# Kernel optimization log

Measured on AMD Instinct MI355X. Metric: run time of the kernel, lower is better.

The kernel has to match this reference:

```python
import jax, jax.numpy as jnp
import numpy as np

N, F, DE = 768, 64, 32
H0, H1, H2, OUT = 64, 64, 128, 1  # hidden_dim=[64,64,128], output_dim=1


def _mlp(x, Wa, ba, Wb, bb):
    # two Dense layers with relu, as in the repo's MLP
    h = jax.nn.relu(x @ Wa + ba)
    return jax.nn.relu(h @ Wb + bb)


def _edge_conv_e(A, x, e, Wa, ba, Wb, bb):
    # EdgeConvE: per-edge message MLP([x_i, x_j - x_i, e_ij]) aggregated
    # over neighbors j weighted by the (binary) adjacency.
    n = x.shape[0]
    xi = jnp.broadcast_to(x[:, None, :], (n, n, x.shape[1]))  # [N,N,F]
    xj = jnp.broadcast_to(x[None, :, :], (n, n, x.shape[1]))  # [N,N,F]
    feat = jnp.concatenate([xi, xj - xi, e], axis=-1)         # [N,N,2F+De]
    m = _mlp(feat, Wa, ba, Wb, bb)                            # [N,N,H]
    return jnp.einsum('ij,ijh->ih', A, m)                     # scatter-sum over j


def setup_inputs() -> dict:
    key = jax.random.key(0)
    ks = jax.random.split(key, 16)
    adj = (jax.random.uniform(ks[0], (N, N)) < 0.05).astype(jnp.float32)
    x = jax.random.normal(ks[1], (N, F), dtype=jnp.float32)
    e = jax.random.normal(ks[2], (N, N, DE), dtype=jnp.float32)
    s = 0.05
    d_in1 = 2 * F + DE          # 160
    d_in2 = 2 * H0 + DE         # 160
    return {
        'ajacency': adj,
        'node_features': x,
        'edge_attributes': e,
        'W1a': jax.random.normal(ks[3], (d_in1, H0)) * s, 'b1a': jnp.zeros((H0,)),
        'W1b': jax.random.normal(ks[4], (H0, H0)) * s,    'b1b': jnp.zeros((H0,)),
        'W2a': jax.random.normal(ks[5], (d_in2, H1)) * s, 'b2a': jnp.zeros((H1,)),
        'W2b': jax.random.normal(ks[6], (H1, H0)) * s,    'b2b': jnp.zeros((H0,)),
        'W3': jax.random.normal(ks[7], (H0, H2)) * s,     'b3': jnp.zeros((H2,)),
        'W4': jax.random.normal(ks[8], (H2, OUT)) * s,    'b4': jnp.zeros((OUT,)),
    }


def reference(ajacency, node_features, edge_attributes,
              W1a, b1a, W1b, b1b, W2a, b2a, W2b, b2b, W3, b3, W4, b4):
    x = _edge_conv_e(ajacency, node_features, edge_attributes, W1a, b1a, W1b, b1b)
    x = _edge_conv_e(ajacency, x, edge_attributes, W2a, b2a, W2b, b2b)
    x = jax.nn.relu(x @ W3 + b3)
    return jax.nn.sigmoid(x @ W4 + b4)  # [N, OUT]
```

## Files before the change

### kernel.cpp

```cpp
#include <hip/hip_runtime.h>
#include <math.h>


#define NN 768
#define FF 64
#define DE 32
#define HH 64
#define CAP 128
#define SH1S 72

using bf16x8 = __attribute__((ext_vector_type(8))) short;
using f32x4  = __attribute__((ext_vector_type(4))) float;

__device__ __forceinline__ short f2b(float f) {
  unsigned u = __float_as_uint(f);
  return (short)((u + 0x7fffu + ((u >> 16) & 1u)) >> 16);
}

__device__ __forceinline__ void phaseB(
    const short* sh1b, const short* __restrict__ Wbp,
    const float* __restrict__ bb, float* xrow, int c, int lane, int wv)
{
  if (c > 0) {
    const int nt = (c + 15) >> 4;
    const int q = lane >> 4, n = lane & 15;
    bf16x8 b0 = *(const bf16x8*)(Wbp + (((wv * 2 + 0) * 4 + q) * 16 + n) * 8);
    bf16x8 b1 = *(const bf16x8*)(Wbp + (((wv * 2 + 1) * 4 + q) * 16 + n) * 8);
    const float bias = bb[wv * 16 + n];
    float s = 0.0f;
    for (int rt = 0; rt < nt; ++rt) {
      const short* sa = sh1b + (rt * 16 + n) * SH1S + q * 8;
      bf16x8 a0 = *(const bf16x8*)(sa);
      bf16x8 a1 = *(const bf16x8*)(sa + 32);
      f32x4 acc = {0.f, 0.f, 0.f, 0.f};
      acc = __builtin_amdgcn_mfma_f32_16x16x32_bf16(a0, b0, acc, 0, 0, 0);
      acc = __builtin_amdgcn_mfma_f32_16x16x32_bf16(a1, b1, acc, 0, 0, 0);
#pragma unroll
      for (int reg = 0; reg < 4; ++reg) {
        const int row = rt * 16 + q * 4 + reg;
        const float v = fmaxf(acc[reg] + bias, 0.0f);
        s += (row < c) ? v : 0.0f;
      }
    }
    s += __shfl_down(s, 32);
    s += __shfl_down(s, 16);
    if (lane < 16) xrow[wv * 16 + lane] = s;
  } else {
    if (lane < 16) xrow[wv * 16 + lane] = 0.0f;
  }
}

__device__ __forceinline__ void phaseA(
    int i, int c, const int* s_j, const float* __restrict__ e,
    const float* __restrict__ U, const float* __restrict__ V,
    const short* __restrict__ Wep, short (*esb)[DE], short* sh1b,
    int tid, int lane, int wv)
{
  for (int slot = tid >> 3; slot < c; slot += 32) {
    const int j = s_j[slot];
    float4 f = ((const float4*)(e + ((size_t)i * NN + j) * DE))[tid & 7];
    short4 s4 = { f2b(f.x), f2b(f.y), f2b(f.z), f2b(f.w) };
    *(short4*)(&esb[slot][(tid & 7) * 4]) = s4;
  }

  const int q = lane >> 4, n = lane & 15;
  const int ch = wv * 16 + n;
  bf16x8 bwe = *(const bf16x8*)(Wep + ((wv * 4 + q) * 16 + n) * 8);
  const float u_ch = (c > 0) ? U[(i << 6) + ch] : 0.0f;
  __syncthreads();

  const int nt = (c + 15) >> 4;
  for (int rt = 0; rt < nt; ++rt) {
    bf16x8 a = *(const bf16x8*)(&esb[rt * 16 + n][q * 8]);
    f32x4 P = {0.f, 0.f, 0.f, 0.f};
    P = __builtin_amdgcn_mfma_f32_16x16x32_bf16(a, bwe, P, 0, 0, 0);
#pragma unroll
    for (int reg = 0; reg < 4; ++reg) {
      const int slot = rt * 16 + q * 4 + reg;
      short val = 0;
      if (slot < c) {
        const int j = s_j[slot];
        val = f2b(fmaxf(u_ch + V[(j << 6) + ch] + P[reg], 0.0f));
      }
      sh1b[slot * SH1S + ch] = val;
    }
  }
  __syncthreads();
}

__global__ __launch_bounds__(256) void scan_kernel(
    const float* __restrict__ A, const float* __restrict__ x,
    const float* __restrict__ W, const float* __restrict__ bias,
    const float* __restrict__ We1, const float* __restrict__ We2,
    const float* __restrict__ Wb1, const float* __restrict__ Wb2,
    int* __restrict__ cnt, int* __restrict__ jl,
    float* __restrict__ U, float* __restrict__ V,
    short* __restrict__ Wbp1, short* __restrict__ Wbp2,
    short* __restrict__ We1p, short* __restrict__ We2p)
{
  const int i = blockIdx.x;
  const int tid = threadIdx.x;
  __shared__ int s_cnt;
  __shared__ int s_j[CAP];
  __shared__ float sx[64];
  __shared__ float su[4][64], sv[4][64];

  if (tid == 0) s_cnt = 0;
  __syncthreads();
  if (tid < 64) sx[tid] = x[i * 64 + tid];
  if (tid < NN / 4) {
    float4 a = ((const float4*)(A + i * NN))[tid];
    if (a.x != 0.0f) { int p = atomicAdd(&s_cnt, 1); if (p < CAP) s_j[p] = tid * 4 + 0; }
    if (a.y != 0.0f) { int p = atomicAdd(&s_cnt, 1); if (p < CAP) s_j[p] = tid * 4 + 1; }
    if (a.z != 0.0f) { int p = atomicAdd(&s_cnt, 1); if (p < CAP) s_j[p] = tid * 4 + 2; }
    if (a.w != 0.0f) { int p = atomicAdd(&s_cnt, 1); if (p < CAP) s_j[p] = tid * 4 + 3; }
  }

  if (i < 2) {
    const float* srcb = (i == 0) ? Wb1 : Wb2;
    short* dstb = (i == 0) ? Wbp1 : Wbp2;
    for (int L = tid; L < 4096; L += 256) {
      const int j = L & 7, n = (L >> 3) & 15, quad = (L >> 7) & 3;
      const int kb = (L >> 9) & 1, ct = L >> 10;
      dstb[L] = f2b(srcb[(kb * 32 + quad * 8 + j) * 64 + ct * 16 + n]);
    }
    const float* srce = (i == 0) ? We1 : We2;
    short* dste = (i == 0) ? We1p : We2p;
    for (int L = tid; L < 2048; L += 256) {
      const int j = L & 7, n = (L >> 3) & 15, q = (L >> 7) & 3, ct = L >> 9;
      dste[L] = f2b(srce[(q * 8 + j) * 64 + ct * 16 + n]);
    }
  }
  __syncthreads();
  const int c = min(s_cnt, CAP);

  const int c64 = tid & 63, sg = tid >> 6;
  {
    float u = 0.0f, v = 0.0f;
#pragma unroll
    for (int t = 0; t < 16; ++t) {
      const int d = sg * 16 + t;
      const float xv = sx[d];
      const float wxi = W[d * 64 + c64];
      const float wxj = W[(64 + d) * 64 + c64];
      u = fmaf(xv, wxi - wxj, u);
      v = fmaf(xv, wxj, v);
    }
    su[sg][c64] = u; sv[sg][c64] = v;
  }
  __syncthreads();

  if (tid < 64) {
    U[i * 64 + tid] = su[0][tid] + su[1][tid] + su[2][tid] + su[3][tid] + bias[tid];
    V[i * 64 + tid] = sv[0][tid] + sv[1][tid] + sv[2][tid] + sv[3][tid];
  }
  if (tid == 0) cnt[i] = c;
  for (int t = tid; t < c; t += 256) jl[(i << 7) + t] = s_j[t];
}

__global__ __launch_bounds__(256) void conv1uv2_kernel(
    const int* __restrict__ cnt, const int* __restrict__ jl,
    const float* __restrict__ e,
    const float* __restrict__ U1, const float* __restrict__ V1,
    const short* __restrict__ We1p, const short* __restrict__ Wbp1,
    const float* __restrict__ b1b,
    const float* __restrict__ W2a, const float* __restrict__ b2a,
    float* __restrict__ U2, float* __restrict__ V2)
{
  const int i = blockIdx.x;
  const int tid = threadIdx.x, lane = tid & 63, wv = tid >> 6;
  __shared__ __align__(16) short esb[CAP][DE];
  __shared__ __align__(16) short sh1b[CAP * SH1S];
  __shared__ int s_j[CAP];
  __shared__ float xrow[64];
  __shared__ float su[4][64], sv[4][64];

  const int c = cnt[i];
  for (int t = tid; t < c; t += 256) s_j[t] = jl[(i << 7) + t];
  __syncthreads();

  phaseA(i, c, s_j, e, U1, V1, We1p, esb, sh1b, tid, lane, wv);
  phaseB(sh1b, Wbp1, b1b, xrow, c, lane, wv);
  __syncthreads();

  const int c64 = tid & 63, qr = tid >> 6;
  {
    float u = 0.0f, v = 0.0f;
#pragma unroll
    for (int t = 0; t < 16; ++t) {
      const int d = qr * 16 + t;
      const float xv = xrow[d];
      const float wxi = W2a[d * 64 + c64];
      const float wxj = W2a[(64 + d) * 64 + c64];
      u = fmaf(xv, wxi - wxj, u);
      v = fmaf(xv, wxj, v);
    }
    su[qr][c64] = u; sv[qr][c64] = v;
  }
  __syncthreads();
  if (tid < 64) {
    U2[i * 64 + tid] = su[0][tid] + su[1][tid] + su[2][tid] + su[3][tid] + b2a[tid];
    V2[i * 64 + tid] = sv[0][tid] + sv[1][tid] + sv[2][tid] + sv[3][tid];
  }
}

__global__ __launch_bounds__(256) void conv2head_kernel(
    const int* __restrict__ cnt, const int* __restrict__ jl,
    const float* __restrict__ e,
    const float* __restrict__ U2, const float* __restrict__ V2,
    const short* __restrict__ We2p, const short* __restrict__ Wbp2,
    const float* __restrict__ b2b,
    const float* __restrict__ W3, const float* __restrict__ b3,
    const float* __restrict__ W4, const float* __restrict__ b4,
    float* __restrict__ out)
{
  const int i = blockIdx.x;
  const int tid = threadIdx.x, lane = tid & 63, wv = tid >> 6;
  __shared__ __align__(16) short esb[CAP][DE];
  __shared__ __align__(16) short sh1b[CAP * SH1S];
  __shared__ int s_j[CAP];
  __shared__ float xrow[64];
  __shared__ float sred[2];

  const int c = cnt[i];
  for (int t = tid; t < c; t += 256) s_j[t] = jl[(i << 7) + t];
  __syncthreads();

  phaseA(i, c, s_j, e, U2, V2, We2p, esb, sh1b, tid, lane, wv);
  phaseB(sh1b, Wbp2, b2b, xrow, c, lane, wv);
  __syncthreads();

  if (tid < 128) {
    float p = b3[tid];
#pragma unroll
    for (int cc = 0; cc < 64; ++cc) p = fmaf(xrow[cc], W3[cc * 128 + tid], p);
    p = fmaxf(p, 0.0f);
    float v = p * W4[tid];
    v += __shfl_down(v, 32);
    v += __shfl_down(v, 16);
    v += __shfl_down(v, 8);
    v += __shfl_down(v, 4);
    v += __shfl_down(v, 2);
    v += __shfl_down(v, 1);
    if (lane == 0) sred[wv] = v;
  }
  __syncthreads();
  if (tid == 0) {
    const float z = sred[0] + sred[1] + b4[0];
    out[i] = 1.0f / (1.0f + expf(-z));
  }
}

extern "C" void kernel_launch(void* const* d_in, const int* in_sizes, int n_in,
                              void* d_out, int out_size, void* d_ws, size_t ws_size,
                              hipStream_t stream) {
  const float* A   = (const float*)d_in[0];
  const float* x   = (const float*)d_in[1];
  const float* e   = (const float*)d_in[2];
  const float* W1a = (const float*)d_in[3];
  const float* b1a = (const float*)d_in[4];
  const float* W1b = (const float*)d_in[5];
  const float* b1b = (const float*)d_in[6];
  const float* W2a = (const float*)d_in[7];
  const float* b2a = (const float*)d_in[8];
  const float* W2b = (const float*)d_in[9];
  const float* b2b = (const float*)d_in[10];
  const float* W3  = (const float*)d_in[11];
  const float* b3  = (const float*)d_in[12];
  const float* W4  = (const float*)d_in[13];
  const float* b4  = (const float*)d_in[14];
  float* out = (float*)d_out;

  int*   cnt  = (int*)d_ws;
  int*   jl   = cnt + NN;
  float* U1   = (float*)(jl + NN * CAP);
  float* V1   = U1 + NN * HH;
  float* U2   = V1 + NN * HH;
  float* V2   = U2 + NN * HH;
  short* Wbp1 = (short*)(V2 + NN * HH);
  short* Wbp2 = Wbp1 + 4096;
  short* We1p = Wbp2 + 4096;
  short* We2p = We1p + 2048;

  scan_kernel<<<NN, 256, 0, stream>>>(A, x, W1a, b1a,
                                      W1a + 128 * HH, W2a + 128 * HH,
                                      W1b, W2b,
                                      cnt, jl, U1, V1, Wbp1, Wbp2, We1p, We2p);
  conv1uv2_kernel<<<NN, 256, 0, stream>>>(cnt, jl, e, U1, V1, We1p, Wbp1, b1b,
                                          W2a, b2a, U2, V2);
  conv2head_kernel<<<NN, 256, 0, stream>>>(cnt, jl, e, U2, V2, We2p, Wbp2, b2b,
                                           W3, b3, W4, b4, out);
}
```

Baseline: 149.9 us.

## Split U/V and weight packing into small kernel, fuse adjacency scan into conv1

Computes the first-layer U/V projections and the bf16 weight packing in a separate, smaller kernel of NN/4+2 blocks, with each thread doing a full 64-term dot product. The adjacency scan moves into the first conv kernel, which now writes cnt and jl itself instead of reading them back from global memory. This cuts the dependency on a full 768-block scan pass and removes one round trip of the neighbor list. In exchange each conv1 block does its scan serially before phase A.

```diff
diff --git a/kernel.cpp b/kernel.cpp
--- a/kernel.cpp
+++ b/kernel.cpp
@@ -88,26 +88,74 @@
   __syncthreads();
 }
 
-__global__ __launch_bounds__(256) void scan_kernel(
-    const float* __restrict__ A, const float* __restrict__ x,
-    const float* __restrict__ W, const float* __restrict__ bias,
+__global__ __launch_bounds__(256) void uvpack_kernel(
+    const float* __restrict__ x, const float* __restrict__ W,
+    const float* __restrict__ bias,
     const float* __restrict__ We1, const float* __restrict__ We2,
     const float* __restrict__ Wb1, const float* __restrict__ Wb2,
-    int* __restrict__ cnt, int* __restrict__ jl,
     float* __restrict__ U, float* __restrict__ V,
     short* __restrict__ Wbp1, short* __restrict__ Wbp2,
     short* __restrict__ We1p, short* __restrict__ We2p)
 {
+  const int b = blockIdx.x;
+  const int tid = threadIdx.x;
+
+  if (b >= NN / 4) {
+    const int which = b - NN / 4;
+    const float* srcb = (which == 0) ? Wb1 : Wb2;
+    short* dstb = (which == 0) ? Wbp1 : Wbp2;
+    for (int L = tid; L < 4096; L += 256) {
+      const int j = L & 7, n = (L >> 3) & 15, quad = (L >> 7) & 3;
+      const int kb = (L >> 9) & 1, ct = L >> 10;
+      dstb[L] = f2b(srcb[(kb * 32 + quad * 8 + j) * 64 + ct * 16 + n]);
+    }
+    const float* srce = (which == 0) ? We1 : We2;
+    short* dste = (which == 0) ? We1p : We2p;
+    for (int L = tid; L < 2048; L += 256) {
+      const int j = L & 7, n = (L >> 3) & 15, q = (L >> 7) & 3, ct = L >> 9;
+      dste[L] = f2b(srce[(q * 8 + j) * 64 + ct * 16 + n]);
+    }
+    return;
+  }
+
+  const int rr = tid >> 6, c64 = tid & 63;
+  const int r = b * 4 + rr;
+  __shared__ float sx[4][64];
+  sx[rr][c64] = x[r * 64 + c64];
+  __syncthreads();
+  float u = bias[c64], v = 0.0f;
+#pragma unroll
+  for (int d = 0; d < 64; ++d) {
+    const float xv = sx[rr][d];
+    const float wxi = W[d * 64 + c64];
+    const float wxj = W[(64 + d) * 64 + c64];
+    u = fmaf(xv, wxi - wxj, u);
+    v = fmaf(xv, wxj, v);
+  }
+  U[r * 64 + c64] = u;
+  V[r * 64 + c64] = v;
+}
+
+__global__ __launch_bounds__(256) void scanconv1_kernel(
+    const float* __restrict__ A, const float* __restrict__ e,
+    const float* __restrict__ U1, const float* __restrict__ V1,
+    const short* __restrict__ We1p, const short* __restrict__ Wbp1,
+    const float* __restrict__ b1b,
+    const float* __restrict__ W2a, const float* __restrict__ b2a,
+    int* __restrict__ cnt, int* __restrict__ jl,
+    float* __restrict__ U2, float* __restrict__ V2)
+{
   const int i = blockIdx.x;
-  const int tid = threadIdx.x;
+  const int tid = threadIdx.x, lane = tid & 63, wv = tid >> 6;
   __shared__ int s_cnt;
   __shared__ int s_j[CAP];
-  __shared__ float sx[64];
+  __shared__ __align__(16) short esb[CAP][DE];
+  __shared__ __align__(16) short sh1b[CAP * SH1S];
+  __shared__ float xrow[64];
   __shared__ float su[4][64], sv[4][64];
 
   if (tid == 0) s_cnt = 0;
   __syncthreads();
-  if (tid < 64) sx[tid] = x[i * 64 + tid];
   if (tid < NN / 4) {
     float4 a = ((const float4*)(A + i * NN))[tid];
     if (a.x != 0.0f) { int p = atomicAdd(&s_cnt, 1); if (p < CAP) s_j[p] = tid * 4 + 0; }
@@ -115,69 +163,10 @@
     if (a.z != 0.0f) { int p = atomicAdd(&s_cnt, 1); if (p < CAP) s_j[p] = tid * 4 + 2; }
     if (a.w != 0.0f) { int p = atomicAdd(&s_cnt, 1); if (p < CAP) s_j[p] = tid * 4 + 3; }
   }
-
-  if (i < 2) {
-    const float* srcb = (i == 0) ? Wb1 : Wb2;
-    short* dstb = (i == 0) ? Wbp1 : Wbp2;
-    for (int L = tid; L < 4096; L += 256) {
-      const int j = L & 7, n = (L >> 3) & 15, quad = (L >> 7) & 3;
-      const int kb = (L >> 9) & 1, ct = L >> 10;
-      dstb[L] = f2b(srcb[(kb * 32 + quad * 8 + j) * 64 + ct * 16 + n]);
-    }
-    const float* srce = (i == 0) ? We1 : We2;
-    short* dste = (i == 0) ? We1p : We2p;
-    for (int L = tid; L < 2048; L += 256) {
-      const int j = L & 7, n = (L >> 3) & 15, q = (L >> 7) & 3, ct = L >> 9;
-      dste[L] = f2b(srce[(q * 8 + j) * 64 + ct * 16 + n]);
-    }
-  }
   __syncthreads();
   const int c = min(s_cnt, CAP);
-
-  const int c64 = tid & 63, sg = tid >> 6;
-  {
-    float u = 0.0f, v = 0.0f;
-#pragma unroll
-    for (int t = 0; t < 16; ++t) {
-      const int d = sg * 16 + t;
-      const float xv = sx[d];
-      const float wxi = W[d * 64 + c64];
-      const float wxj = W[(64 + d) * 64 + c64];
-      u = fmaf(xv, wxi - wxj, u);
-      v = fmaf(xv, wxj, v);
-    }
-    su[sg][c64] = u; sv[sg][c64] = v;
-  }
-  __syncthreads();
-
-  if (tid < 64) {
-    U[i * 64 + tid] = su[0][tid] + su[1][tid] + su[2][tid] + su[3][tid] + bias[tid];
-    V[i * 64 + tid] = sv[0][tid] + sv[1][tid] + sv[2][tid] + sv[3][tid];
-  }
   if (tid == 0) cnt[i] = c;
   for (int t = tid; t < c; t += 256) jl[(i << 7) + t] = s_j[t];
-}
-
-__global__ __launch_bounds__(256) void conv1uv2_kernel(
-    const int* __restrict__ cnt, const int* __restrict__ jl,
-    const float* __restrict__ e,
-    const float* __restrict__ U1, const float* __restrict__ V1,
-    const short* __restrict__ We1p, const short* __restrict__ Wbp1,
-    const float* __restrict__ b1b,
-    const float* __restrict__ W2a, const float* __restrict__ b2a,
-    float* __restrict__ U2, float* __restrict__ V2)
-{
-  const int i = blockIdx.x;
-  const int tid = threadIdx.x, lane = tid & 63, wv = tid >> 6;
-  __shared__ __align__(16) short esb[CAP][DE];
-  __shared__ __align__(16) short sh1b[CAP * SH1S];
-  __shared__ int s_j[CAP];
-  __shared__ float xrow[64];
-  __shared__ float su[4][64], sv[4][64];
-
-  const int c = cnt[i];
-  for (int t = tid; t < c; t += 256) s_j[t] = jl[(i << 7) + t];
-  __syncthreads();
 
   phaseA(i, c, s_j, e, U1, V1, We1p, esb, sh1b, tid, lane, wv);
   phaseB(sh1b, Wbp1, b1b, xrow, c, lane, wv);
@@ -282,12 +271,12 @@
   short* We1p = Wbp2 + 4096;
   short* We2p = We1p + 2048;
 
-  scan_kernel<<<NN, 256, 0, stream>>>(A, x, W1a, b1a,
-                                      W1a + 128 * HH, W2a + 128 * HH,
-                                      W1b, W2b,
-                                      cnt, jl, U1, V1, Wbp1, Wbp2, We1p, We2p);
-  conv1uv2_kernel<<<NN, 256, 0, stream>>>(cnt, jl, e, U1, V1, We1p, Wbp1, b1b,
-                                          W2a, b2a, U2, V2);
+  uvpack_kernel<<<NN / 4 + 2, 256, 0, stream>>>(x, W1a, b1a,
+                                                W1a + 128 * HH, W2a + 128 * HH,
+                                                W1b, W2b,
+                                                U1, V1, Wbp1, Wbp2, We1p, We2p);
+  scanconv1_kernel<<<NN, 256, 0, stream>>>(A, e, U1, V1, We1p, Wbp1, b1b,
+                                           W2a, b2a, cnt, jl, U2, V2);
   conv2head_kernel<<<NN, 256, 0, stream>>>(cnt, jl, e, U2, V2, We2p, Wbp2, b2b,
                                            W3, b3, W4, b4, out);
 }
```

Result: faster. 146.4 us (-2.3%).
